# Optimization experiments

Measured on AMD Instinct MI355X. Metric: run time of the kernel, lower is better.

Reference implementation:

```python
import jax, jax.numpy as jnp
import numpy as np

B, T, S, D = 32, 1024, 1024, 512
VOCAB = 1000
INSERT_TOK = jnp.array([1, 2], dtype=jnp.int64)


def setup_inputs() -> dict:
    key = jax.random.key(0)
    k1, k2, k3, k4, k5 = jax.random.split(key, 5)
    input_var = jax.random.randint(k1, (B, T), 0, VOCAB, dtype=jnp.int64)
    output = jax.random.normal(k2, (B, T, D), jnp.float32)
    context = jax.random.normal(k3, (B, S, D), jnp.float32)
    # nn.Linear(2*dim, dim): weight [D, 2D], bias [D]
    W = jax.random.normal(k4, (D, 2 * D), jnp.float32) / np.sqrt(2 * D)
    b = jax.random.normal(k5, (D,), jnp.float32) * 0.01
    return {"input_var": input_var, "output": output, "context": context,
            "di": 0, "W": W, "b": b}


def _hard_align(input_var, src_len):
    """Replicates the python double-loop: sequential 'inserted' counter per batch.
    Returns (j, valid): j[b,i] = column of the 1.0 in attn row i (torch negative
    indices wrapped), valid[b,i] = whether row i gets any 1.0 at all."""
    bsz, tgt_len = input_var.shape
    flags = jnp.isin(input_var, INSERT_TOK)  # [B,T] is token an insert token

    def step(inserted, xi):
        i, flag = xi  # i: scalar position, flag: [B]
        cond = (src_len >= i - inserted)                    # gate, per batch
        ins2 = inserted + jnp.where(cond & flag, 1, 0)      # increment before write
        j = i - ins2 - 1
        j = jnp.where(j < 0, j + src_len, j)                # torch negative-index wrap
        return ins2, (j, cond)

    idxs = jnp.arange(1, tgt_len, dtype=jnp.int32)
    init = jnp.zeros((bsz,), jnp.int32)  # init_inserted()
    _, (j_rows, valid) = jax.lax.scan(step, init, (idxs, flags[:, 1:].T))
    j_rows = j_rows.T      # [B,T-1]
    valid = valid.T        # [B,T-1]
    # row 0: attn[b,0,0] = 1.0 always
    j_full = jnp.concatenate([jnp.zeros((bsz, 1), j_rows.dtype), j_rows], axis=1)
    valid_full = jnp.concatenate([jnp.ones((bsz, 1), bool), valid], axis=1)
    return j_full, valid_full


def reference(input_var, output, context, di, W, b):
    bsz, tgt_len, hid = output.shape
    src_len = context.shape[1]
    j, valid = _hard_align(input_var, src_len)              # [B,T], [B,T]
    vf = valid[:, :, None].astype(output.dtype)
    # hard one-hot attention matrix (as the module materializes it)
    attn = jax.nn.one_hot(j, src_len, dtype=output.dtype) * vf  # [B,T,S]
    # mix = bmm(attn, context) == masked gather of context rows
    mix = jnp.take_along_axis(context, j[:, :, None].astype(jnp.int32), axis=1) * vf
    combined = jnp.concatenate([mix, output], axis=-1)      # [B,T,2D]
    out = jnp.tanh(combined @ W.T + b)                      # [B,T,D]
    return out, attn
```

## Files before the change

### kernel.cpp

```cpp
#include <hip/hip_runtime.h>
#include <hip/hip_bf16.h>

#define B_ 32
#define T_ 1024
#define S_ 1024
#define D_ 512
#define M_ (B_*T_)
#define N_ D_
#define K_ (2*D_)

typedef __attribute__((ext_vector_type(8))) short bf16x8;
typedef __attribute__((ext_vector_type(4))) float f32x4;

__device__ inline unsigned short f2bf(float x) {
    union { float f; unsigned u; } v; v.f = x;
    unsigned r = v.u + 0x7FFFu + ((v.u >> 16) & 1u);
    return (unsigned short)(r >> 16);
}

__device__ inline unsigned cvt2bf(float lo, float hi) {
#if __has_builtin(__builtin_amdgcn_cvt_pk_bf16_f32)
    typedef __attribute__((ext_vector_type(2))) __bf16 bf2;
    union { bf2 v; unsigned u; } r;
    r.v = __builtin_amdgcn_cvt_pk_bf16_f32(lo, hi);
    return r.u;
#else
    return (unsigned)f2bf(lo) | ((unsigned)f2bf(hi) << 16);
#endif
}

__device__ inline float fast_tanh(float x) {
#if __has_builtin(__builtin_amdgcn_exp2f) && __has_builtin(__builtin_amdgcn_rcpf)
    const float e = __builtin_amdgcn_exp2f(x * 2.885390082f);
    const float r = __builtin_amdgcn_rcpf(e + 1.0f);
    return 1.0f - 2.0f * r;
#else
    return tanhf(x);
#endif
}

__global__ void align_kernel(const int* __restrict__ iv, int* __restrict__ jbuf) {
    const int b = blockIdx.x;
    const int lane = threadIdx.x;
    const int* row = iv + b * T_;
    int f[16];
    int local = 0;
    const int t0 = lane * 16;
    #pragma unroll
    for (int q = 0; q < 16; ++q) {
        const int t = t0 + q;
        const int tok = row[t];
        const int fl = (t > 0 && (tok == 1 || tok == 2)) ? 1 : 0;
        f[q] = fl;
        local += fl;
    }
    int incl = local;
    #pragma unroll
    for (int off = 1; off < 64; off <<= 1) {
        const int up = __shfl_up(incl, off, 64);
        if (lane >= off) incl += up;
    }
    int run = incl - local;
    #pragma unroll
    for (int q = 0; q < 16; ++q) {
        const int t = t0 + q;
        run += f[q];
        int j;
        if (t == 0) {
            j = 0;
        } else {
            j = t - run - 1;
            if (j < 0) j += S_;
        }
        jbuf[b * T_ + t] = j;
    }
}

__global__ void pack_w(const float* __restrict__ W, unsigned short* __restrict__ Wbf) {
    const int idx = blockIdx.x * blockDim.x + threadIdx.x;
    const f32x4 a = ((const f32x4*)W)[idx * 2];
    const f32x4 c = ((const f32x4*)W)[idx * 2 + 1];
    union { bf16x8 v; unsigned u[4]; } pk;
    pk.u[0] = cvt2bf(a[0], a[1]); pk.u[1] = cvt2bf(a[2], a[3]);
    pk.u[2] = cvt2bf(c[0], c[1]); pk.u[3] = cvt2bf(c[2], c[3]);
    *(bf16x8*)(Wbf + (size_t)idx * 8) = pk.v;
}

#define BM 128
#define BN 128
#define BK 64
#define NGEMM ((M_ / BM) * (N_ / BN))
#define NATTN 512

__global__ __launch_bounds__(256, 4)
void gemm_attn(const unsigned short* __restrict__ Wbf,
               const float* __restrict__ bias,
               float* __restrict__ out,
               float* __restrict__ attn,
               const float* __restrict__ ctx,
               const float* __restrict__ outp,
               const int* __restrict__ jbuf) {
    const int bx = blockIdx.x;
    const int tid = threadIdx.x;

    if (bx < NATTN) {
        const int m0 = bx * 64;
        #pragma unroll 4
        for (int r = 0; r < 64; ++r) {
            const int row = m0 + r;
            const int j = jbuf[row];
            f32x4 v = {0.f, 0.f, 0.f, 0.f};
            if ((j >> 2) == tid) v[j & 3] = 1.0f;
            ((f32x4*)(attn + (size_t)row * S_))[tid] = v;
        }
        return;
    }

    __shared__ unsigned short As[BM * BK];
    __shared__ unsigned short Bs[BN * BK];

    const int gbx  = bx - NATTN;
    const int lane = tid & 63;
    const int wave = tid >> 6;
    const int wm = wave >> 1, wn = wave & 1;
    const int l16 = lane & 15, quad = lane >> 4;

    const int bm = gbx & 255;
    const int bn = gbx >> 8;
    const int mBase = bm * BM;
    const int nBase = bn * BN;

    const int kc   = tid & 7;
    const int rsub = tid >> 3;
    const int sw   = kc ^ (rsub & 7);
    const float* actx[4];
    const float* aout[4];
    #pragma unroll
    for (int it = 0; it < 4; ++it) {
        const int r = it * 32 + rsub;
        const int m = mBase + r;
        const int jm = jbuf[m];
        actx[it] = ctx + ((size_t)((m >> 10) * S_ + jm)) * D_ + kc * 8;
        aout[it] = outp + (size_t)m * D_ - D_ + kc * 8;
    }

    f32x4 acc[4][4] = {};

    for (int ko = 0; ko < K_; ko += BK) {
        f32x4 fa[4][2];
        #pragma unroll
        for (int it = 0; it < 4; ++it) {
            const float* src = (ko < D_) ? (actx[it] + ko) : (aout[it] + ko);
            fa[it][0] = ((const f32x4*)src)[0];
            fa[it][1] = ((const f32x4*)src)[1];
        }
        #pragma unroll
        for (int it = 0; it < 4; ++it) {
            const int chunk = it * 256 + tid;
            const int row = chunk >> 3;
            const int kcb = chunk & 7;
            const int gk8 = (kcb ^ (row & 7)) * 8;
            const unsigned short* gB = Wbf + (size_t)(nBase + row) * K_ + ko + gk8;
            __builtin_amdgcn_global_load_lds(
                (const __attribute__((address_space(1))) void*)gB,
                (__attribute__((address_space(3))) void*)(Bs + chunk * 8), 16, 0, 0);
        }
        #pragma unroll
        for (int it = 0; it < 4; ++it) {
            union { bf16x8 v; unsigned u[4]; } pk;
            pk.u[0] = cvt2bf(fa[it][0][0], fa[it][0][1]);
            pk.u[1] = cvt2bf(fa[it][0][2], fa[it][0][3]);
            pk.u[2] = cvt2bf(fa[it][1][0], fa[it][1][1]);
            pk.u[3] = cvt2bf(fa[it][1][2], fa[it][1][3]);
            *(bf16x8*)&As[(it * 256 + rsub * 8 + sw) * 8] = pk.v;
        }
        __syncthreads();

        #pragma unroll
        for (int ks = 0; ks < 2; ++ks) {
            bf16x8 af[4], bfr[4];
            #pragma unroll
            for (int mt = 0; mt < 4; ++mt) {
                const int r = wm * 64 + mt * 16 + l16;
                const int q = ks * 4 + quad;
                af[mt] = *(const bf16x8*)&As[(r * 8 + (q ^ (r & 7))) * 8];
            }
            #pragma unroll
            for (int nt = 0; nt < 4; ++nt) {
                const int r = wn * 64 + nt * 16 + l16;
                const int q = ks * 4 + quad;
                bfr[nt] = *(const bf16x8*)&Bs[(r * 8 + (q ^ (r & 7))) * 8];
            }
            #pragma unroll
            for (int mt = 0; mt < 4; ++mt)
                #pragma unroll
                for (int nt = 0; nt < 4; ++nt)
                    acc[mt][nt] = __builtin_amdgcn_mfma_f32_16x16x32_bf16(
                        af[mt], bfr[nt], acc[mt][nt], 0, 0, 0);
        }
        __syncthreads();
    }

    #pragma unroll
    for (int nt = 0; nt < 4; ++nt) {
        const int n = nBase + wn * 64 + nt * 16 + l16;
        const float bv = bias[n];
        #pragma unroll
        for (int mt = 0; mt < 4; ++mt) {
            #pragma unroll
            for (int r = 0; r < 4; ++r) {
                const int m = mBase + wm * 64 + mt * 16 + quad * 4 + r;
                out[(size_t)m * N_ + n] = fast_tanh(acc[mt][nt][r] + bv);
            }
        }
    }
}

extern "C" void kernel_launch(void* const* d_in, const int* in_sizes, int n_in,
                              void* d_out, int out_size, void* d_ws, size_t ws_size,
                              hipStream_t stream) {
    const int*   iv   = (const int*)d_in[0];
    const float* outp = (const float*)d_in[1];
    const float* ctx  = (const float*)d_in[2];
    const float* W    = (const float*)d_in[4];
    const float* bias = (const float*)d_in[5];

    float* out  = (float*)d_out;
    float* attn = out + (size_t)M_ * N_;

    int* jbuf = (int*)d_ws;
    unsigned short* Wbf = (unsigned short*)((char*)d_ws + (size_t)M_ * 4);

    align_kernel<<<B_, 64, 0, stream>>>(iv, jbuf);
    pack_w<<<(N_ * K_ / 8) / 256, 256, 0, stream>>>(W, Wbf);
    gemm_attn<<<NGEMM + NATTN, 256, 0, stream>>>(Wbf, bias, out, attn, ctx, outp, jbuf);
}
```

Before: 357.6 us.

## Double-buffer GEMM LDS tiles with register prefetch and manual waitcnt pipelining

```diff
diff --git a/kernel.cpp b/kernel.cpp
--- a/kernel.cpp
+++ b/kernel.cpp
@@ -89,10 +89,12 @@
 #define BM 128
 #define BN 128
 #define BK 64
+#define NIT (K_ / BK)
+#define KMAX (K_ - BK)
 #define NGEMM ((M_ / BM) * (N_ / BN))
 #define NATTN 512
 
-__global__ __launch_bounds__(256, 4)
+__global__ __launch_bounds__(256, 2)
 void gemm_attn(const unsigned short* __restrict__ Wbf,
                const float* __restrict__ bias,
                float* __restrict__ out,
@@ -111,13 +113,13 @@
             const int j = jbuf[row];
             f32x4 v = {0.f, 0.f, 0.f, 0.f};
             if ((j >> 2) == tid) v[j & 3] = 1.0f;
-            ((f32x4*)(attn + (size_t)row * S_))[tid] = v;
+            __builtin_nontemporal_store(v, ((f32x4*)(attn + (size_t)row * S_)) + tid);
         }
         return;
     }
 
-    __shared__ unsigned short As[BM * BK];
-    __shared__ unsigned short Bs[BN * BK];
+    __shared__ unsigned short As[2][BM * BK];
+    __shared__ unsigned short Bs[2][BN * BK];
 
     const int gbx  = bx - NATTN;
     const int lane = tid & 63;
@@ -145,61 +147,117 @@
     }
 
     f32x4 acc[4][4] = {};
-
-    for (int ko = 0; ko < K_; ko += BK) {
-        f32x4 fa[4][2];
-        #pragma unroll
-        for (int it = 0; it < 4; ++it) {
-            const float* src = (ko < D_) ? (actx[it] + ko) : (aout[it] + ko);
-            fa[it][0] = ((const f32x4*)src)[0];
-            fa[it][1] = ((const f32x4*)src)[1];
-        }
-        #pragma unroll
-        for (int it = 0; it < 4; ++it) {
-            const int chunk = it * 256 + tid;
-            const int row = chunk >> 3;
-            const int kcb = chunk & 7;
-            const int gk8 = (kcb ^ (row & 7)) * 8;
-            const unsigned short* gB = Wbf + (size_t)(nBase + row) * K_ + ko + gk8;
-            __builtin_amdgcn_global_load_lds(
-                (const __attribute__((address_space(1))) void*)gB,
-                (__attribute__((address_space(3))) void*)(Bs + chunk * 8), 16, 0, 0);
-        }
-        #pragma unroll
-        for (int it = 0; it < 4; ++it) {
-            union { bf16x8 v; unsigned u[4]; } pk;
-            pk.u[0] = cvt2bf(fa[it][0][0], fa[it][0][1]);
-            pk.u[1] = cvt2bf(fa[it][0][2], fa[it][0][3]);
-            pk.u[2] = cvt2bf(fa[it][1][0], fa[it][1][1]);
-            pk.u[3] = cvt2bf(fa[it][1][2], fa[it][1][3]);
-            *(bf16x8*)&As[(it * 256 + rsub * 8 + sw) * 8] = pk.v;
-        }
-        __syncthreads();
-
-        #pragma unroll
-        for (int ks = 0; ks < 2; ++ks) {
-            bf16x8 af[4], bfr[4];
-            #pragma unroll
-            for (int mt = 0; mt < 4; ++mt) {
-                const int r = wm * 64 + mt * 16 + l16;
-                const int q = ks * 4 + quad;
-                af[mt] = *(const bf16x8*)&As[(r * 8 + (q ^ (r & 7))) * 8];
-            }
-            #pragma unroll
-            for (int nt = 0; nt < 4; ++nt) {
-                const int r = wn * 64 + nt * 16 + l16;
-                const int q = ks * 4 + quad;
-                bfr[nt] = *(const bf16x8*)&Bs[(r * 8 + (q ^ (r & 7))) * 8];
-            }
-            #pragma unroll
-            for (int mt = 0; mt < 4; ++mt)
-                #pragma unroll
-                for (int nt = 0; nt < 4; ++nt)
-                    acc[mt][nt] = __builtin_amdgcn_mfma_f32_16x16x32_bf16(
-                        af[mt], bfr[nt], acc[mt][nt], 0, 0, 0);
-        }
-        __syncthreads();
-    }
+    f32x4 fa0[4][2], fa1[4][2];
+
+#define LOAD_A(FA, KO) do {                                                    \
+    const int _koa = (KO);                                                     \
+    _Pragma("unroll")                                                          \
+    for (int _it = 0; _it < 4; ++_it) {                                        \
+        const float* _src = (_koa < D_) ? (actx[_it] + _koa) : (aout[_it] + _koa); \
+        FA[_it][0] = ((const f32x4*)_src)[0];                                  \
+        FA[_it][1] = ((const f32x4*)_src)[1];                                  \
+    }                                                                          \
+} while (0)
+
+#define DMA_B(PP, KO) do {                                                     \
+    const int _kob = (KO);                                                     \
+    _Pragma("unroll")                                                          \
+    for (int _it = 0; _it < 4; ++_it) {                                        \
+        const int _chunk = _it * 256 + tid;                                    \
+        const int _row = _chunk >> 3;                                          \
+        const int _kcb = _chunk & 7;                                           \
+        const int _gk8 = (_kcb ^ (_row & 7)) * 8;                              \
+        const unsigned short* _gB = Wbf + (size_t)(nBase + _row) * K_ + _kob + _gk8; \
+        __builtin_amdgcn_global_load_lds(                                      \
+            (const __attribute__((address_space(1))) void*)_gB,                \
+            (__attribute__((address_space(3))) void*)(&Bs[PP][_chunk * 8]), 16, 0, 0); \
+    }                                                                          \
+} while (0)
+
+#define STAGE_A(PP, FA) do {                                                   \
+    _Pragma("unroll")                                                          \
+    for (int _it = 0; _it < 4; ++_it) {                                        \
+        union { bf16x8 v; unsigned u[4]; } _pk;                                \
+        _pk.u[0] = cvt2bf(FA[_it][0][0], FA[_it][0][1]);                       \
+        _pk.u[1] = cvt2bf(FA[_it][0][2], FA[_it][0][3]);                       \
+        _pk.u[2] = cvt2bf(FA[_it][1][0], FA[_it][1][1]);                       \
+        _pk.u[3] = cvt2bf(FA[_it][1][2], FA[_it][1][3]);                       \
+        *(bf16x8*)&As[PP][(_it * 256 + rsub * 8 + sw) * 8] = _pk.v;            \
+    }                                                                          \
+} while (0)
+
+#define MFMA_PH(PP) do {                                                       \
+    _Pragma("unroll")                                                          \
+    for (int _ks = 0; _ks < 2; ++_ks) {                                        \
+        bf16x8 _af[4], _bfr[4];                                                \
+        _Pragma("unroll")                                                      \
+        for (int _mt = 0; _mt < 4; ++_mt) {                                    \
+            const int _r = wm * 64 + _mt * 16 + l16;                           \
+            const int _q = _ks * 4 + quad;                                     \
+            _af[_mt] = *(const bf16x8*)&As[PP][(_r * 8 + (_q ^ (_r & 7))) * 8]; \
+        }                                                                      \
+        _Pragma("unroll")                                                      \
+        for (int _nt = 0; _nt < 4; ++_nt) {                                    \
+            const int _r = wn * 64 + _nt * 16 + l16;                           \
+            const int _q = _ks * 4 + quad;                                     \
+            _bfr[_nt] = *(const bf16x8*)&Bs[PP][(_r * 8 + (_q ^ (_r & 7))) * 8]; \
+        }                                                                      \
+        _Pragma("unroll")                                                      \
+        for (int _mt = 0; _mt < 4; ++_mt)                                      \
+            _Pragma("unroll")                                                  \
+            for (int _nt = 0; _nt < 4; ++_nt)                                  \
+                acc[_mt][_nt] = __builtin_amdgcn_mfma_f32_16x16x32_bf16(       \
+                    _af[_mt], _bfr[_nt], acc[_mt][_nt], 0, 0, 0);              \
+    }                                                                          \
+} while (0)
+
+    LOAD_A(fa0, 0);
+    DMA_B(0, 0);
+    __builtin_amdgcn_sched_barrier(0);
+    LOAD_A(fa1, BK);
+    __builtin_amdgcn_sched_barrier(0);
+    STAGE_A(0, fa0);
+    asm volatile("s_waitcnt vmcnt(8) lgkmcnt(0)" ::: "memory");
+    __builtin_amdgcn_sched_barrier(0);
+    __builtin_amdgcn_s_barrier();
+
+    #pragma unroll 1
+    for (int i = 0; i < NIT; i += 2) {
+        const int ko = i * BK;
+        DMA_B(1, ko + BK);
+        __builtin_amdgcn_sched_barrier(0);
+        {
+            const int _ka = (ko + 2 * BK > KMAX) ? KMAX : ko + 2 * BK;
+            LOAD_A(fa0, _ka);
+        }
+        __builtin_amdgcn_sched_barrier(0);
+        STAGE_A(1, fa1);
+        MFMA_PH(0);
+        asm volatile("s_waitcnt vmcnt(8) lgkmcnt(0)" ::: "memory");
+        __builtin_amdgcn_sched_barrier(0);
+        __builtin_amdgcn_s_barrier();
+
+        {
+            const int _kb = (ko + 2 * BK > KMAX) ? KMAX : ko + 2 * BK;
+            DMA_B(0, _kb);
+        }
+        __builtin_amdgcn_sched_barrier(0);
+        {
+            const int _kcl = (ko + 3 * BK > KMAX) ? KMAX : ko + 3 * BK;
+            LOAD_A(fa1, _kcl);
+        }
+        __builtin_amdgcn_sched_barrier(0);
+        STAGE_A(0, fa0);
+        MFMA_PH(1);
+        asm volatile("s_waitcnt vmcnt(8) lgkmcnt(0)" ::: "memory");
+        __builtin_amdgcn_sched_barrier(0);
+        __builtin_amdgcn_s_barrier();
+    }
+
+#undef LOAD_A
+#undef DMA_B
+#undef STAGE_A
+#undef MFMA_PH
 
     #pragma unroll
     for (int nt = 0; nt < 4; ++nt) {
@@ -210,7 +268,8 @@
             #pragma unroll
             for (int r = 0; r < 4; ++r) {
                 const int m = mBase + wm * 64 + mt * 16 + quad * 4 + r;
-                out[(size_t)m * N_ + n] = fast_tanh(acc[mt][nt][r] + bv);
+                const float val = fast_tanh(acc[mt][nt][r] + bv);
+                __builtin_nontemporal_store(val, &out[(size_t)m * N_ + n]);
             }
         }
     }
```

New measurement: 352.0 us. Within noise of the previous version (-1.6%).

## Pre-pack gathered activations to bf16 and stream both GEMM operands via LDS loads

Applied to the files above, without the earlier changes.

```diff
diff --git a/kernel.cpp b/kernel.cpp
--- a/kernel.cpp
+++ b/kernel.cpp
@@ -86,6 +86,33 @@
     *(bf16x8*)(Wbf + (size_t)idx * 8) = pk.v;
 }
 
+__global__ __launch_bounds__(256)
+void prep_kernel(const float* __restrict__ ctx, const float* __restrict__ outp,
+                 const int* __restrict__ jbuf, unsigned short* __restrict__ Abf) {
+    const int bx = blockIdx.x;
+    const int wave = threadIdx.x >> 6;
+    const int lane = threadIdx.x & 63;
+    #pragma unroll 2
+    for (int r = 0; r < 8; ++r) {
+        const int m = bx * 32 + wave * 8 + r;
+        const int j = jbuf[m];
+        const int b = m >> 10;
+        const float* s1 = ctx + ((size_t)(b * S_ + j)) * D_ + lane * 8;
+        const float* s2 = outp + (size_t)m * D_ + lane * 8;
+        const f32x4 a0 = ((const f32x4*)s1)[0];
+        const f32x4 a1 = ((const f32x4*)s1)[1];
+        const f32x4 c0 = ((const f32x4*)s2)[0];
+        const f32x4 c1 = ((const f32x4*)s2)[1];
+        union { bf16x8 v; unsigned u[4]; } p1, p2;
+        p1.u[0] = cvt2bf(a0[0], a0[1]); p1.u[1] = cvt2bf(a0[2], a0[3]);
+        p1.u[2] = cvt2bf(a1[0], a1[1]); p1.u[3] = cvt2bf(a1[2], a1[3]);
+        p2.u[0] = cvt2bf(c0[0], c0[1]); p2.u[1] = cvt2bf(c0[2], c0[3]);
+        p2.u[2] = cvt2bf(c1[0], c1[1]); p2.u[3] = cvt2bf(c1[2], c1[3]);
+        *(bf16x8*)(Abf + (size_t)m * K_ + lane * 8)       = p1.v;
+        *(bf16x8*)(Abf + (size_t)m * K_ + D_ + lane * 8)  = p2.v;
+    }
+}
+
 #define BM 128
 #define BN 128
 #define BK 64
@@ -93,86 +120,54 @@
 #define NATTN 512
 
 __global__ __launch_bounds__(256, 4)
-void gemm_attn(const unsigned short* __restrict__ Wbf,
-               const float* __restrict__ bias,
-               float* __restrict__ out,
-               float* __restrict__ attn,
-               const float* __restrict__ ctx,
-               const float* __restrict__ outp,
-               const int* __restrict__ jbuf) {
-    const int bx = blockIdx.x;
-    const int tid = threadIdx.x;
-
-    if (bx < NATTN) {
-        const int m0 = bx * 64;
-        #pragma unroll 4
-        for (int r = 0; r < 64; ++r) {
-            const int row = m0 + r;
-            const int j = jbuf[row];
-            f32x4 v = {0.f, 0.f, 0.f, 0.f};
-            if ((j >> 2) == tid) v[j & 3] = 1.0f;
-            ((f32x4*)(attn + (size_t)row * S_))[tid] = v;
-        }
-        return;
-    }
-
+void gemm_lin(const unsigned short* __restrict__ Abf,
+              const unsigned short* __restrict__ Wbf,
+              const float* __restrict__ bias,
+              float* __restrict__ out) {
     __shared__ unsigned short As[BM * BK];
     __shared__ unsigned short Bs[BN * BK];
 
-    const int gbx  = bx - NATTN;
+    const int gbx = blockIdx.x;
+    const int tid = threadIdx.x;
     const int lane = tid & 63;
     const int wave = tid >> 6;
     const int wm = wave >> 1, wn = wave & 1;
     const int l16 = lane & 15, quad = lane >> 4;
 
-    const int bm = gbx & 255;
-    const int bn = gbx >> 8;
+    const int xcd = gbx & 7;
+    const int bn  = (gbx >> 3) & 3;
+    const int bm  = ((gbx >> 5) << 3) | xcd;
     const int mBase = bm * BM;
     const int nBase = bn * BN;
 
-    const int kc   = tid & 7;
-    const int rsub = tid >> 3;
-    const int sw   = kc ^ (rsub & 7);
-    const float* actx[4];
-    const float* aout[4];
+    const unsigned short* aSrc[4];
+    const unsigned short* bSrc[4];
     #pragma unroll
     for (int it = 0; it < 4; ++it) {
-        const int r = it * 32 + rsub;
-        const int m = mBase + r;
-        const int jm = jbuf[m];
-        actx[it] = ctx + ((size_t)((m >> 10) * S_ + jm)) * D_ + kc * 8;
-        aout[it] = outp + (size_t)m * D_ - D_ + kc * 8;
+        const int chunk = it * 256 + tid;
+        const int row = chunk >> 3;
+        const int g   = chunk & 7;
+        const int gk8 = (g ^ (row & 7)) * 8;
+        aSrc[it] = Abf + (size_t)(mBase + row) * K_ + gk8;
+        bSrc[it] = Wbf + (size_t)(nBase + row) * K_ + gk8;
     }
 
     f32x4 acc[4][4] = {};
 
     for (int ko = 0; ko < K_; ko += BK) {
-        f32x4 fa[4][2];
-        #pragma unroll
-        for (int it = 0; it < 4; ++it) {
-            const float* src = (ko < D_) ? (actx[it] + ko) : (aout[it] + ko);
-            fa[it][0] = ((const f32x4*)src)[0];
-            fa[it][1] = ((const f32x4*)src)[1];
-        }
         #pragma unroll
         for (int it = 0; it < 4; ++it) {
             const int chunk = it * 256 + tid;
-            const int row = chunk >> 3;
-            const int kcb = chunk & 7;
-            const int gk8 = (kcb ^ (row & 7)) * 8;
-            const unsigned short* gB = Wbf + (size_t)(nBase + row) * K_ + ko + gk8;
             __builtin_amdgcn_global_load_lds(
-                (const __attribute__((address_space(1))) void*)gB,
+                (const __attribute__((address_space(1))) void*)(aSrc[it] + ko),
+                (__attribute__((address_space(3))) void*)(As + chunk * 8), 16, 0, 0);
+        }
+        #pragma unroll
+        for (int it = 0; it < 4; ++it) {
+            const int chunk = it * 256 + tid;
+            __builtin_amdgcn_global_load_lds(
+                (const __attribute__((address_space(1))) void*)(bSrc[it] + ko),
                 (__attribute__((address_space(3))) void*)(Bs + chunk * 8), 16, 0, 0);
-        }
-        #pragma unroll
-        for (int it = 0; it < 4; ++it) {
-            union { bf16x8 v; unsigned u[4]; } pk;
-            pk.u[0] = cvt2bf(fa[it][0][0], fa[it][0][1]);
-            pk.u[1] = cvt2bf(fa[it][0][2], fa[it][0][3]);
-            pk.u[2] = cvt2bf(fa[it][1][0], fa[it][1][1]);
-            pk.u[3] = cvt2bf(fa[it][1][2], fa[it][1][3]);
-            *(bf16x8*)&As[(it * 256 + rsub * 8 + sw) * 8] = pk.v;
         }
         __syncthreads();
 
@@ -213,6 +208,21 @@
                 out[(size_t)m * N_ + n] = fast_tanh(acc[mt][nt][r] + bv);
             }
         }
+    }
+}
+
+__global__ __launch_bounds__(256)
+void attn_fill(float* __restrict__ attn, const int* __restrict__ jbuf) {
+    const int bx = blockIdx.x;
+    const int tid = threadIdx.x;
+    const int m0 = bx * 64;
+    #pragma unroll 4
+    for (int r = 0; r < 64; ++r) {
+        const int row = m0 + r;
+        const int j = jbuf[row];
+        f32x4 v = {0.f, 0.f, 0.f, 0.f};
+        if ((j >> 2) == tid) v[j & 3] = 1.0f;
+        ((f32x4*)(attn + (size_t)row * S_))[tid] = v;
     }
 }
 
@@ -231,7 +241,11 @@
     int* jbuf = (int*)d_ws;
     unsigned short* Wbf = (unsigned short*)((char*)d_ws + (size_t)M_ * 4);
 
+    unsigned short* Abf = (unsigned short*)attn;
+
     align_kernel<<<B_, 64, 0, stream>>>(iv, jbuf);
     pack_w<<<(N_ * K_ / 8) / 256, 256, 0, stream>>>(W, Wbf);
-    gemm_attn<<<NGEMM + NATTN, 256, 0, stream>>>(Wbf, bias, out, attn, ctx, outp, jbuf);
-}
+    prep_kernel<<<M_ / 32, 256, 0, stream>>>(ctx, outp, jbuf, Abf);
+    gemm_lin<<<NGEMM, 256, 0, stream>>>(Abf, Wbf, bias, out);
+    attn_fill<<<NATTN, 256, 0, stream>>>(attn, jbuf);
+}
```

Measured after the change: 377.0 us. 5.4% more time.
